# Kernel tuning notes

Measured on AMD Instinct MI355X. Metric: run time of the kernel, lower is better.

## Reference

```python
import jax, jax.numpy as jnp
import numpy as np

B, T, D, N = 4, 2048, 1024, 16

def setup_inputs() -> dict:
    key = jax.random.key(0)
    ks = jax.random.split(key, 6)
    scale = 0.02
    return {
        'x': jax.random.normal(ks[0], (B, T, D), dtype=jnp.float32),
        'Wd': jax.random.normal(ks[1], (D, D), dtype=jnp.float32) * (1.0 / np.sqrt(D)),
        'bd': jnp.zeros((D,), dtype=jnp.float32),
        'a_log': jax.random.normal(ks[2], (D, N), dtype=jnp.float32) * scale,
        'b_param': jax.random.normal(ks[3], (D, N), dtype=jnp.float32) * scale,
        'Wo': jax.random.normal(ks[4], (D, D), dtype=jnp.float32) * (1.0 / np.sqrt(D)),
        'bo': jnp.zeros((D,), dtype=jnp.float32),
    }

def reference(x, Wd, bd, a_log, b_param, Wo, bo):
    # delta: [B,T,D]
    delta = jax.nn.softplus(jnp.einsum('btd,ed->bte', x, Wd) + bd)
    a_pos = jax.nn.softplus(a_log) + 1e-4  # [D,N]

    def step(state, inputs):
        x_t, delta_t = inputs  # [B,D], [B,D]
        dt = delta_t[..., None]                      # [B,D,1]
        a_bar = jnp.exp(-dt * a_pos)                 # [B,D,N]
        state = a_bar * state + (dt * b_param) * x_t[..., None]
        return state, state.sum(axis=-1)             # y_t: [B,D]

    init = jnp.zeros((B, D, N), dtype=x.dtype)
    xs = (jnp.swapaxes(x, 0, 1), jnp.swapaxes(delta, 0, 1))  # [T,B,D]
    _, y = jax.lax.scan(step, init, xs)              # y: [T,B,D]
    y = jnp.swapaxes(y, 0, 1)                        # [B,T,D]
    return jnp.einsum('btd,ed->bte', y, Wo) + bo
```

## Files before the change

kernel.cpp:

```cpp
#include <hip/hip_runtime.h>
#include <hip/hip_bf16.h>

#define B_ 4
#define T_ 2048
#define D_ 1024
#define N_ 16
#define TCH 32
#define NCH 64

#define GM 8192
#define GK 1024
#define GN 1024

typedef __attribute__((ext_vector_type(4))) float f32x4;
typedef __attribute__((ext_vector_type(8))) short short8;
typedef unsigned int u32;
typedef unsigned short u16;

#if defined(__has_builtin)
#if __has_builtin(__builtin_amdgcn_exp2f)
#define EXP2(x) __builtin_amdgcn_exp2f(x)
#else
#define EXP2(x) exp2f(x)
#endif
#else
#define EXP2(x) exp2f(x)
#endif

__device__ __forceinline__ float softplus_f(float v) {
    return v > 20.f ? v : log1pf(__expf(v));
}

__device__ __forceinline__ u16 f2bf(float f) {
    u32 u = __float_as_uint(f);
    u32 r = (u + 0x7fffu + ((u >> 16) & 1u)) >> 16;
    return (u16)r;
}

__global__ __launch_bounds__(256) void cvt_f32_bf16(const float* __restrict__ in,
                                                    u16* __restrict__ out, int n4) {
    int i = blockIdx.x * 256 + threadIdx.x;
    if (i >= n4) return;
    float4 v = ((const float4*)in)[i];
    ushort4 o;
    o.x = f2bf(v.x); o.y = f2bf(v.y); o.z = f2bf(v.z); o.w = f2bf(v.w);
    ((ushort4*)out)[i] = o;
}

template <int ACT>
__global__ __launch_bounds__(512, 8) void gemm_bt(const u16* __restrict__ A,
                                                  const u16* __restrict__ Bw,
                                                  const float* __restrict__ bias,
                                                  float* __restrict__ C) {
    __shared__ __align__(16) u16 sA[64 * 64];
    __shared__ __align__(16) u16 sB[128 * 64];
    const int tid = threadIdx.x;
    const int wid = tid >> 6;
    const int lane = tid & 63;

    const int wg = blockIdx.x;
    const int xcd = wg & 7;
    const int jj = wg >> 3;
    const int bx = xcd * 16 + (jj & 15);
    const int by = jj >> 4;
    const int m0 = bx * 64;
    const int n0 = by * 128;
    const int wm = wid >> 2;
    const int wn = wid & 3;

    const int lrow = lane >> 3;
    const int slot = lane & 7;
    const int ksw = (slot ^ lrow) << 3;

    const u16* aP  = A  + (size_t)(m0 + wid * 8 + lrow) * GK + ksw;
    const u16* bP0 = Bw + (size_t)(n0 + wid * 8 + lrow) * GK + ksw;
    const u16* bP1 = Bw + (size_t)(n0 + (wid + 8) * 8 + lrow) * GK + ksw;

    const int wOff = wid * 1024 + lrow * 128 + slot * 16;
    char* const wA  = (char*)sA + wOff;
    char* const wB  = (char*)sB + wOff;

    const int fr = lane & 15;
    const int g = lane >> 4;
    const int xorv = (fr & 7) << 4;
    const char* const rA0 = (const char*)sA + (wm * 32 + fr) * 128 + ((g * 16) ^ xorv);
    const char* const rA1 = (const char*)sA + (wm * 32 + fr) * 128 + ((64 + g * 16) ^ xorv);
    const char* const rB0 = (const char*)sB + (wn * 32 + fr) * 128 + ((g * 16) ^ xorv);
    const char* const rB1 = (const char*)sB + (wn * 32 + fr) * 128 + ((64 + g * 16) ^ xorv);

    short8 ra, rb0, rb1;
    f32x4 acc[2][2] = {};

    ra  = *(const short8*)(aP);
    rb0 = *(const short8*)(bP0);
    rb1 = *(const short8*)(bP1);
    *(short8*)(wA)        = ra;
    *(short8*)(wB)        = rb0;
    *(short8*)(wB + 8192) = rb1;
    ra  = *(const short8*)(aP + 64);
    rb0 = *(const short8*)(bP0 + 64);
    rb1 = *(const short8*)(bP1 + 64);
    asm volatile("s_waitcnt lgkmcnt(0)" ::: "memory");
    __builtin_amdgcn_s_barrier();
    asm volatile("" ::: "memory");

    #pragma unroll
    for (int t = 0; t < GK / 64; ++t) {
        #pragma unroll
        for (int kk = 0; kk < 2; ++kk) {
            const char* bA = kk ? rA1 : rA0;
            const char* bB = kk ? rB1 : rB0;
            short8 af[2], bf[2];
            #pragma unroll
            for (int f = 0; f < 2; ++f)
                af[f] = *(const short8*)(bA + f * 2048);
            #pragma unroll
            for (int f = 0; f < 2; ++f)
                bf[f] = *(const short8*)(bB + f * 2048);
            __builtin_amdgcn_s_setprio(1);
            #pragma unroll
            for (int i = 0; i < 2; ++i)
                #pragma unroll
                for (int j2 = 0; j2 < 2; ++j2)
                    acc[i][j2] = __builtin_amdgcn_mfma_f32_16x16x32_bf16(af[i], bf[j2],
                                                                         acc[i][j2], 0, 0, 0);
            __builtin_amdgcn_s_setprio(0);
        }
        if (t + 1 < GK / 64) {
            asm volatile("s_waitcnt lgkmcnt(0)" ::: "memory");
            __builtin_amdgcn_s_barrier();
            asm volatile("" ::: "memory");
            *(short8*)(wA)        = ra;
            *(short8*)(wB)        = rb0;
            *(short8*)(wB + 8192) = rb1;
            asm volatile("s_waitcnt lgkmcnt(0)" ::: "memory");
            __builtin_amdgcn_s_barrier();
            asm volatile("" ::: "memory");
            if (t + 2 < GK / 64) {
                ra  = *(const short8*)(aP  + (t + 2) * 64);
                rb0 = *(const short8*)(bP0 + (t + 2) * 64);
                rb1 = *(const short8*)(bP1 + (t + 2) * 64);
            }
        }
    }

    const int cl = lane & 15;
    const int rg = (lane >> 4) * 4;
    #pragma unroll
    for (int j2 = 0; j2 < 2; ++j2) {
        const int col = n0 + wn * 32 + j2 * 16 + cl;
        const float bv = bias[col];
        #pragma unroll
        for (int i = 0; i < 2; ++i) {
            #pragma unroll
            for (int r = 0; r < 4; ++r) {
                const int rowg = m0 + wm * 32 + i * 16 + rg + r;
                float v = acc[i][j2][r] + bv;
                if (ACT) v = softplus_f(v);
                C[(size_t)rowg * GN + col] = v;
            }
        }
    }
}

__global__ __launch_bounds__(256) void scan_p1(const float* __restrict__ delta,
                                               const float* __restrict__ x,
                                               const float* __restrict__ a_log,
                                               float* __restrict__ S,
                                               float* __restrict__ dtsum) {
    const int gid = blockIdx.x * 256 + threadIdx.x;
    const int lane = gid & 63;
    const int w = gid >> 6;
    const int dw = w & 31;
    const int cb = w >> 5;
    const int d = dw * 32 + (lane & 31);
    const int half = lane >> 5;
    const int b = cb & (B_ - 1);
    const int c = cb >> 2;

    float an2[8];
    {
        const float4* a4 = (const float4*)&a_log[d * N_ + half * 8];
        float4 a0 = a4[0], a1 = a4[1];
        an2[0] = (softplus_f(a0.x) + 1e-4f) * 1.44269504f;
        an2[1] = (softplus_f(a0.y) + 1e-4f) * 1.44269504f;
        an2[2] = (softplus_f(a0.z) + 1e-4f) * 1.44269504f;
        an2[3] = (softplus_f(a0.w) + 1e-4f) * 1.44269504f;
        an2[4] = (softplus_f(a1.x) + 1e-4f) * 1.44269504f;
        an2[5] = (softplus_f(a1.y) + 1e-4f) * 1.44269504f;
        an2[6] = (softplus_f(a1.z) + 1e-4f) * 1.44269504f;
        an2[7] = (softplus_f(a1.w) + 1e-4f) * 1.44269504f;
    }

    float s[8];
    #pragma unroll
    for (int n = 0; n < 8; ++n) s[n] = 0.f;
    float dts = 0.f;

    const size_t base = ((size_t)b * T_ + (size_t)c * TCH) * D_ + d;
    for (int i = 0; i < TCH; ++i) {
        const float dt = delta[base + (size_t)i * D_];
        const float xv = x[base + (size_t)i * D_];
        const float dtx = dt * xv;
        dts += dt;
        #pragma unroll
        for (int n = 0; n < 8; ++n) {
            const float ab = EXP2(-dt * an2[n]);
            s[n] = fmaf(ab, s[n], dtx);
        }
    }

    float4* So = (float4*)&S[((size_t)cb * D_ + d) * N_ + half * 8];
    So[0] = make_float4(s[0], s[1], s[2], s[3]);
    So[1] = make_float4(s[4], s[5], s[6], s[7]);
    if (half == 0) dtsum[(size_t)cb * D_ + d] = dts;
}

__global__ __launch_bounds__(256) void scan_p2(const float* __restrict__ S,
                                               const float* __restrict__ dtsum,
                                               const float* __restrict__ a_log,
                                               float* __restrict__ carry_out) {
    const int gid = blockIdx.x * 256 + threadIdx.x;
    const int n = gid & 15;
    const int d = (gid >> 4) & (D_ - 1);
    const int b = gid >> 14;
    const float an2 = (softplus_f(a_log[d * N_ + n]) + 1e-4f) * 1.44269504f;
    float carry = 0.f;
    for (int c = 0; c < NCH; ++c) {
        const size_t cb = (size_t)c * B_ + b;
        const size_t idx = (cb * D_ + d) * N_ + n;
        carry_out[idx] = carry;
        const float dts = dtsum[cb * D_ + d];
        const float P = EXP2(-dts * an2);
        carry = fmaf(P, carry, S[idx]);
    }
}

__global__ __launch_bounds__(256) void scan_p3(const float* __restrict__ delta,
                                               const float* __restrict__ x,
                                               const float* __restrict__ a_log,
                                               const float* __restrict__ b_param,
                                               const float* __restrict__ carry_in,
                                               u16* __restrict__ y) {
    const int gid = blockIdx.x * 256 + threadIdx.x;
    const int lane = gid & 63;
    const int w = gid >> 6;
    const int dw = w & 31;
    const int cb = w >> 5;
    const int d = dw * 32 + (lane & 31);
    const int half = lane >> 5;
    const int b = cb & (B_ - 1);
    const int c = cb >> 2;

    float an2[8], bp[8];
    {
        const float4* a4 = (const float4*)&a_log[d * N_ + half * 8];
        const float4* b4 = (const float4*)&b_param[d * N_ + half * 8];
        float4 a0 = a4[0], a1 = a4[1];
        float4 v0 = b4[0], v1 = b4[1];
        an2[0] = (softplus_f(a0.x) + 1e-4f) * 1.44269504f;
        an2[1] = (softplus_f(a0.y) + 1e-4f) * 1.44269504f;
        an2[2] = (softplus_f(a0.z) + 1e-4f) * 1.44269504f;
        an2[3] = (softplus_f(a0.w) + 1e-4f) * 1.44269504f;
        an2[4] = (softplus_f(a1.x) + 1e-4f) * 1.44269504f;
        an2[5] = (softplus_f(a1.y) + 1e-4f) * 1.44269504f;
        an2[6] = (softplus_f(a1.z) + 1e-4f) * 1.44269504f;
        an2[7] = (softplus_f(a1.w) + 1e-4f) * 1.44269504f;
        bp[0] = v0.x; bp[1] = v0.y; bp[2] = v0.z; bp[3] = v0.w;
        bp[4] = v1.x; bp[5] = v1.y; bp[6] = v1.z; bp[7] = v1.w;
    }

    float s[8];
    {
        const float4* ci = (const float4*)&carry_in[((size_t)cb * D_ + d) * N_ + half * 8];
        float4 c0 = ci[0], c1 = ci[1];
        s[0] = c0.x; s[1] = c0.y; s[2] = c0.z; s[3] = c0.w;
        s[4] = c1.x; s[5] = c1.y; s[6] = c1.z; s[7] = c1.w;
    }

    const size_t base = ((size_t)b * T_ + (size_t)c * TCH) * D_ + d;
    for (int i = 0; i < TCH; ++i) {
        const float dt = delta[base + (size_t)i * D_];
        const float xv = x[base + (size_t)i * D_];
        const float dtx = dt * xv;
        float acc = 0.f;
        #pragma unroll
        for (int n = 0; n < 8; ++n) {
            const float ab = EXP2(-dt * an2[n]);
            s[n] = fmaf(ab, s[n], dtx);
            acc = fmaf(bp[n], s[n], acc);
        }
        const float tot = acc + __shfl_xor(acc, 32);
        if (half == 0) y[base + (size_t)i * D_] = f2bf(tot);
    }
}

extern "C" void kernel_launch(void* const* d_in, const int* in_sizes, int n_in,
                              void* d_out, int out_size, void* d_ws, size_t ws_size,
                              hipStream_t stream) {
    const float* x      = (const float*)d_in[0];
    const float* Wd     = (const float*)d_in[1];
    const float* bd     = (const float*)d_in[2];
    const float* a_log  = (const float*)d_in[3];
    const float* b_par  = (const float*)d_in[4];
    const float* Wo     = (const float*)d_in[5];
    const float* bo     = (const float*)d_in[6];
    float* out = (float*)d_out;

    char* ws = (char*)d_ws;
    u16*   xbf     = (u16*)(ws);
    float* carry   = (float*)(ws);
    float* S       = (float*)(ws + 16777216);
    u16*   ybf     = (u16*)(ws + 16777216);
    float* delta   = (float*)(ws + 33554432);
    u16*   wdbf    = (u16*)(ws + 67108864);
    u16*   wobf    = (u16*)(ws + 69206016);
    float* dtsum   = (float*)(ws + 71303168);
    (void)in_sizes; (void)n_in; (void)out_size; (void)ws_size;

    const int M = B_ * T_;

    cvt_f32_bf16<<<(M * D_ / 4 + 255) / 256, 256, 0, stream>>>(x, xbf, M * D_ / 4);
    cvt_f32_bf16<<<(D_ * D_ / 4 + 255) / 256, 256, 0, stream>>>(Wd, wdbf, D_ * D_ / 4);
    cvt_f32_bf16<<<(D_ * D_ / 4 + 255) / 256, 256, 0, stream>>>(Wo, wobf, D_ * D_ / 4);

    gemm_bt<1><<<(GM / 64) * (GN / 128), 512, 0, stream>>>(xbf, wdbf, bd, delta);

    scan_p1<<<NCH * B_ * D_ * 2 / 256, 256, 0, stream>>>(delta, x, a_log, S, dtsum);
    scan_p2<<<B_ * D_ * N_ / 256, 256, 0, stream>>>(S, dtsum, a_log, carry);
    scan_p3<<<NCH * B_ * D_ * 2 / 256, 256, 0, stream>>>(delta, x, a_log, b_par, carry, ybf);

    gemm_bt<0><<<(GM / 64) * (GN / 128), 512, 0, stream>>>(ybf, wobf, bo, out);
}
```

Baseline: 171.1 us.

## Double-buffer GEMM LDS tiles and feed scans bf16 delta and x

The GEMM now keeps two LDS buffers and writes the next tile while computing the current one, which cuts the two barriers per k-step down to one. The delta GEMM writes bf16 output, and both scan passes read bf16 delta and bf16 x (reusing the converted x) instead of fp32. This halves the memory traffic of the scan kernels and the delta store. The cost is extra LDS per block, which lowers the occupancy bound from 8 to 6, and lower precision for delta and x inside the recurrence.

```diff
diff --git a/kernel.cpp b/kernel.cpp
--- a/kernel.cpp
+++ b/kernel.cpp
@@ -36,6 +36,9 @@
     u32 r = (u + 0x7fffu + ((u >> 16) & 1u)) >> 16;
     return (u16)r;
 }
+__device__ __forceinline__ float bf2f(u16 v) {
+    return __uint_as_float(((u32)v) << 16);
+}
 
 __global__ __launch_bounds__(256) void cvt_f32_bf16(const float* __restrict__ in,
                                                     u16* __restrict__ out, int n4) {
@@ -47,13 +50,13 @@
     ((ushort4*)out)[i] = o;
 }
 
-template <int ACT>
-__global__ __launch_bounds__(512, 8) void gemm_bt(const u16* __restrict__ A,
+template <int ACT, int OBF>
+__global__ __launch_bounds__(512, 6) void gemm_bt(const u16* __restrict__ A,
                                                   const u16* __restrict__ Bw,
                                                   const float* __restrict__ bias,
-                                                  float* __restrict__ C) {
-    __shared__ __align__(16) u16 sA[64 * 64];
-    __shared__ __align__(16) u16 sB[128 * 64];
+                                                  void* __restrict__ Cout) {
+    __shared__ __align__(16) u16 sA[2][64 * 64];
+    __shared__ __align__(16) u16 sB[2][128 * 64];
     const int tid = threadIdx.x;
     const int wid = tid >> 6;
     const int lane = tid & 63;
@@ -77,16 +80,16 @@
     const u16* bP1 = Bw + (size_t)(n0 + (wid + 8) * 8 + lrow) * GK + ksw;
 
     const int wOff = wid * 1024 + lrow * 128 + slot * 16;
-    char* const wA  = (char*)sA + wOff;
-    char* const wB  = (char*)sB + wOff;
+    char* const wA = (char*)sA[0] + wOff;
+    char* const wB = (char*)sB[0] + wOff;
 
     const int fr = lane & 15;
     const int g = lane >> 4;
     const int xorv = (fr & 7) << 4;
-    const char* const rA0 = (const char*)sA + (wm * 32 + fr) * 128 + ((g * 16) ^ xorv);
-    const char* const rA1 = (const char*)sA + (wm * 32 + fr) * 128 + ((64 + g * 16) ^ xorv);
-    const char* const rB0 = (const char*)sB + (wn * 32 + fr) * 128 + ((g * 16) ^ xorv);
-    const char* const rB1 = (const char*)sB + (wn * 32 + fr) * 128 + ((64 + g * 16) ^ xorv);
+    const char* const rA0 = (const char*)sA[0] + (wm * 32 + fr) * 128 + ((g * 16) ^ xorv);
+    const char* const rA1 = (const char*)sA[0] + (wm * 32 + fr) * 128 + ((64 + g * 16) ^ xorv);
+    const char* const rB0 = (const char*)sB[0] + (wn * 32 + fr) * 128 + ((g * 16) ^ xorv);
+    const char* const rB1 = (const char*)sB[0] + (wn * 32 + fr) * 128 + ((64 + g * 16) ^ xorv);
 
     short8 ra, rb0, rb1;
     f32x4 acc[2][2] = {};
@@ -94,9 +97,9 @@
     ra  = *(const short8*)(aP);
     rb0 = *(const short8*)(bP0);
     rb1 = *(const short8*)(bP1);
-    *(short8*)(wA)        = ra;
-    *(short8*)(wB)        = rb0;
-    *(short8*)(wB + 8192) = rb1;
+    *(short8*)(wA)         = ra;
+    *(short8*)(wB)         = rb0;
+    *(short8*)(wB + 8192)  = rb1;
     ra  = *(const short8*)(aP + 64);
     rb0 = *(const short8*)(bP0 + 64);
     rb1 = *(const short8*)(bP1 + 64);
@@ -106,10 +109,22 @@
 
     #pragma unroll
     for (int t = 0; t < GK / 64; ++t) {
+        if (t + 1 < GK / 64) {
+            const int nb = (t + 1) & 1;
+            *(short8*)(wA + nb * 8192)          = ra;
+            *(short8*)(wB + nb * 16384)         = rb0;
+            *(short8*)(wB + nb * 16384 + 8192)  = rb1;
+        }
+        if (t + 2 < GK / 64) {
+            ra  = *(const short8*)(aP  + (t + 2) * 64);
+            rb0 = *(const short8*)(bP0 + (t + 2) * 64);
+            rb1 = *(const short8*)(bP1 + (t + 2) * 64);
+        }
+        const int cb = t & 1;
         #pragma unroll
         for (int kk = 0; kk < 2; ++kk) {
-            const char* bA = kk ? rA1 : rA0;
-            const char* bB = kk ? rB1 : rB0;
+            const char* bA = (kk ? rA1 : rA0) + cb * 8192;
+            const char* bB = (kk ? rB1 : rB0) + cb * 16384;
             short8 af[2], bf[2];
             #pragma unroll
             for (int f = 0; f < 2; ++f)
@@ -126,22 +141,9 @@
                                                                          acc[i][j2], 0, 0, 0);
             __builtin_amdgcn_s_setprio(0);
         }
-        if (t + 1 < GK / 64) {
-            asm volatile("s_waitcnt lgkmcnt(0)" ::: "memory");
-            __builtin_amdgcn_s_barrier();
-            asm volatile("" ::: "memory");
-            *(short8*)(wA)        = ra;
-            *(short8*)(wB)        = rb0;
-            *(short8*)(wB + 8192) = rb1;
-            asm volatile("s_waitcnt lgkmcnt(0)" ::: "memory");
-            __builtin_amdgcn_s_barrier();
-            asm volatile("" ::: "memory");
-            if (t + 2 < GK / 64) {
-                ra  = *(const short8*)(aP  + (t + 2) * 64);
-                rb0 = *(const short8*)(bP0 + (t + 2) * 64);
-                rb1 = *(const short8*)(bP1 + (t + 2) * 64);
-            }
-        }
+        asm volatile("s_waitcnt lgkmcnt(0)" ::: "memory");
+        __builtin_amdgcn_s_barrier();
+        asm volatile("" ::: "memory");
     }
 
     const int cl = lane & 15;
@@ -157,14 +159,15 @@
                 const int rowg = m0 + wm * 32 + i * 16 + rg + r;
                 float v = acc[i][j2][r] + bv;
                 if (ACT) v = softplus_f(v);
-                C[(size_t)rowg * GN + col] = v;
+                if (OBF) ((u16*)Cout)[(size_t)rowg * GN + col] = f2bf(v);
+                else     ((float*)Cout)[(size_t)rowg * GN + col] = v;
             }
         }
     }
 }
 
-__global__ __launch_bounds__(256) void scan_p1(const float* __restrict__ delta,
-                                               const float* __restrict__ x,
+__global__ __launch_bounds__(256) void scan_p1(const u16* __restrict__ delta,
+                                               const u16* __restrict__ x,
                                                const float* __restrict__ a_log,
                                                float* __restrict__ S,
                                                float* __restrict__ dtsum) {
@@ -199,8 +202,8 @@
 
     const size_t base = ((size_t)b * T_ + (size_t)c * TCH) * D_ + d;
     for (int i = 0; i < TCH; ++i) {
-        const float dt = delta[base + (size_t)i * D_];
-        const float xv = x[base + (size_t)i * D_];
+        const float dt = bf2f(delta[base + (size_t)i * D_]);
+        const float xv = bf2f(x[base + (size_t)i * D_]);
         const float dtx = dt * xv;
         dts += dt;
         #pragma unroll
@@ -236,8 +239,8 @@
     }
 }
 
-__global__ __launch_bounds__(256) void scan_p3(const float* __restrict__ delta,
-                                               const float* __restrict__ x,
+__global__ __launch_bounds__(256) void scan_p3(const u16* __restrict__ delta,
+                                               const u16* __restrict__ x,
                                                const float* __restrict__ a_log,
                                                const float* __restrict__ b_param,
                                                const float* __restrict__ carry_in,
@@ -280,8 +283,8 @@
 
     const size_t base = ((size_t)b * T_ + (size_t)c * TCH) * D_ + d;
     for (int i = 0; i < TCH; ++i) {
-        const float dt = delta[base + (size_t)i * D_];
-        const float xv = x[base + (size_t)i * D_];
+        const float dt = bf2f(delta[base + (size_t)i * D_]);
+        const float xv = bf2f(x[base + (size_t)i * D_]);
         const float dtx = dt * xv;
         float acc = 0.f;
         #pragma unroll
@@ -309,10 +312,10 @@
 
     char* ws = (char*)d_ws;
     u16*   xbf     = (u16*)(ws);
-    float* carry   = (float*)(ws);
     float* S       = (float*)(ws + 16777216);
     u16*   ybf     = (u16*)(ws + 16777216);
-    float* delta   = (float*)(ws + 33554432);
+    u16*   deltabf = (u16*)(ws + 33554432);
+    float* carry   = (float*)(ws + 50331648);
     u16*   wdbf    = (u16*)(ws + 67108864);
     u16*   wobf    = (u16*)(ws + 69206016);
     float* dtsum   = (float*)(ws + 71303168);
@@ -324,11 +327,11 @@
     cvt_f32_bf16<<<(D_ * D_ / 4 + 255) / 256, 256, 0, stream>>>(Wd, wdbf, D_ * D_ / 4);
     cvt_f32_bf16<<<(D_ * D_ / 4 + 255) / 256, 256, 0, stream>>>(Wo, wobf, D_ * D_ / 4);
 
-    gemm_bt<1><<<(GM / 64) * (GN / 128), 512, 0, stream>>>(xbf, wdbf, bd, delta);
-
-    scan_p1<<<NCH * B_ * D_ * 2 / 256, 256, 0, stream>>>(delta, x, a_log, S, dtsum);
+    gemm_bt<1, 1><<<(GM / 64) * (GN / 128), 512, 0, stream>>>(xbf, wdbf, bd, deltabf);
+
+    scan_p1<<<NCH * B_ * D_ * 2 / 256, 256, 0, stream>>>(deltabf, xbf, a_log, S, dtsum);
     scan_p2<<<B_ * D_ * N_ / 256, 256, 0, stream>>>(S, dtsum, a_log, carry);
-    scan_p3<<<NCH * B_ * D_ * 2 / 256, 256, 0, stream>>>(delta, x, a_log, b_par, carry, ybf);
-
-    gemm_bt<0><<<(GM / 64) * (GN / 128), 512, 0, stream>>>(ybf, wobf, bo, out);
-}
+    scan_p3<<<NCH * B_ * D_ * 2 / 256, 256, 0, stream>>>(deltabf, xbf, a_log, b_par, carry, ybf);
+
+    gemm_bt<0, 0><<<(GM / 64) * (GN / 128), 512, 0, stream>>>(ybf, wobf, bo, out);
+}
```

Result: no change. 169.0 us (-1.2%).
